# Performance work log

Measured on AMD Instinct MI355X. Metric: run time of the kernel, lower is better.

## Reference

```python
import jax, jax.numpy as jnp
import numpy as np

B, N, C_IN, C_OUT, K = 2, 8192, 128, 128, 21  # K = num_neighbors + 1 (self)
EPS = 1e-5

def knn_idx(xyz, k):
    # xyz: [B,N,3] -> idx [B,N,k] of k nearest neighbors (self included)
    d2 = jnp.sum(xyz * xyz, axis=-1)  # [B,N]
    dist = d2[:, :, None] + d2[:, None, :] - 2.0 * jnp.einsum('bnd,bmd->bnm', xyz, xyz)
    _, idx = jax.lax.top_k(-dist, k)
    return idx

def group_points(pts, idx):
    # pts [B,N,D], idx [B,N,K] -> [B,N,K,D]
    return jax.vmap(lambda p, i: p[i])(pts, idx)

def group_feats(f, idx):
    # f [B,C,N], idx [B,N,K] -> [B,C,N,K]
    return jax.vmap(lambda ff, i: ff[:, i])(f, idx)

def conv_bn_relu(x, W, g, b, m, v):
    # 1x1 conv (bias=False) + BatchNorm (inference stats) + ReLU
    y = jnp.einsum('oc,bcnk->bonk', W, x)
    inv = g / jnp.sqrt(v + EPS)
    return jax.nn.relu(y * inv[None, :, None, None] + (b - m * inv)[None, :, None, None])

def setup_inputs():
    key = jax.random.key(0)
    ks = jax.random.split(key, 12)
    return {
        'xyz': jax.random.normal(ks[0], (B, N, 3), jnp.float32),
        'f': jax.random.normal(ks[1], (B, C_IN, N), jnp.float32),
        'W_geo': jax.random.normal(ks[2], (C_OUT, 6), jnp.float32) * 0.1,
        'g_geo': jax.random.uniform(ks[3], (C_OUT,), jnp.float32, 0.5, 1.5),
        'b_geo': jax.random.normal(ks[4], (C_OUT,), jnp.float32) * 0.1,
        'm_geo': jax.random.normal(ks[5], (C_OUT,), jnp.float32) * 0.1,
        'v_geo': jax.random.uniform(ks[6], (C_OUT,), jnp.float32, 0.5, 1.5),
        'W_feat': jax.random.normal(ks[7], (C_OUT, 2 * C_IN), jnp.float32) * 0.05,
        'g_feat': jax.random.uniform(ks[8], (C_OUT,), jnp.float32, 0.5, 1.5),
        'b_feat': jax.random.normal(ks[9], (C_OUT,), jnp.float32) * 0.1,
        'm_feat': jax.random.normal(ks[10], (C_OUT,), jnp.float32) * 0.1,
        'v_feat': jax.random.uniform(ks[11], (C_OUT,), jnp.float32, 0.5, 1.5),
    }

def reference(xyz, f, W_geo, g_geo, b_geo, m_geo, v_geo, W_feat, g_feat, b_feat, m_feat, v_feat):
    idx = knn_idx(xyz, K)                                   # [B,N,K]
    grouped_xyz = group_points(xyz, idx)                    # [B,N,K,3]
    xyz_diff = jnp.transpose(grouped_xyz - xyz[:, :, None, :], (0, 3, 1, 2))  # [B,3,N,K]
    center = jnp.broadcast_to(jnp.transpose(xyz, (0, 2, 1))[:, :, :, None], (B, 3, N, K))
    G_geo = jnp.concatenate([center, xyz_diff], axis=1)     # [B,6,N,K]
    grouped_f = group_feats(f, idx)                         # [B,C,N,K]
    center_f = jnp.broadcast_to(f[:, :, :, None], (B, C_IN, N, K))
    G_feat = jnp.concatenate([center_f, grouped_f - center_f], axis=1)  # [B,2C,N,K]
    G_geo = conv_bn_relu(G_geo, W_geo, g_geo, b_geo, m_geo, v_geo)      # [B,C_OUT,N,K]
    G_feat = conv_bn_relu(G_feat, W_feat, g_feat, b_feat, m_feat, v_feat)
    feature = jnp.concatenate([G_geo, G_feat], axis=1)      # [B,2*C_OUT,N,K]
    return jnp.max(feature, axis=-1)                        # [B,2*C_OUT,N]
```

## Files before the change

kernel.cpp:

```cpp
#include <hip/hip_runtime.h>

typedef unsigned int u32;
typedef unsigned long long u64;
typedef unsigned short u16;

#define DEV __device__ __forceinline__

DEV u16 f2bf(float x) {
  u32 u = __float_as_uint(x);
  u32 r = u + 0x7fffu + ((u >> 16) & 1u);
  return (u16)(r >> 16);
}
DEV float bflo(u32 d) { return __uint_as_float(d << 16); }
DEV float bfhi(u32 d) { return __uint_as_float(d & 0xffff0000u); }
DEV u64 sortable64(double f) {
  long long b = __double_as_longlong(f);
  return (u64)b ^ (u64)((b >> 63) | (long long)0x8000000000000000ll);
}
DEV double ddist(double qx, double qy, double qz, double qd2,
                 float mxf, float myf, float mzf) {
  double cx = (double)mxf, cy = (double)myf, cz = (double)mzf;
  double cd2 = cx * cx + cy * cy + cz * cz;
  double dot = cx * qx + cy * qy + cz * qz;
  return (qd2 + cd2) - 2.0 * dot;
}

#define NB 2
#define NN 8192
#define NC 128
#define KK 21
#define MARGIN 1e-3f
#define CT 2048

__global__ __launch_bounds__(256) void k_prep(
    const float* __restrict__ Wf, const float* __restrict__ gf, const float* __restrict__ bf_,
    const float* __restrict__ mf, const float* __restrict__ vf,
    const float* __restrict__ Wg, const float* __restrict__ gg, const float* __restrict__ bg,
    const float* __restrict__ mg, const float* __restrict__ vg,
    u16* __restrict__ Wt, float* __restrict__ beta_f,
    float* __restrict__ Wgu, float* __restrict__ Wgv, float* __restrict__ beta_g) {
  int g = blockIdx.x * 256 + threadIdx.x;
  int c = g >> 8, o = g & 255;
  float val;
  if (o < 128) {
    float inv = gf[o] / sqrtf(vf[o] + 1e-5f);
    val = inv * (Wf[o * 256 + c] - Wf[o * 256 + c + 128]);
  } else {
    int o2 = o - 128;
    float inv = gf[o2] / sqrtf(vf[o2] + 1e-5f);
    val = inv * Wf[o2 * 256 + c + 128];
  }
  Wt[c * 256 + o] = f2bf(val);
  if (g < 128) {
    float inv = gf[g] / sqrtf(vf[g] + 1e-5f);
    beta_f[g] = bf_[g] - mf[g] * inv;
  } else if (g < 256) {
    int oo = g - 128;
    float invg = gg[oo] / sqrtf(vg[oo] + 1e-5f);
#pragma unroll
    for (int d = 0; d < 3; ++d) {
      Wgu[oo * 3 + d] = invg * (Wg[oo * 6 + d] - Wg[oo * 6 + 3 + d]);
      Wgv[oo * 3 + d] = invg * Wg[oo * 6 + 3 + d];
    }
    beta_g[oo] = bg[oo] - mg[oo] * invg;
  }
}

__global__ __launch_bounds__(256) void k_geo(
    const float* __restrict__ xyz, const float* __restrict__ Wgu, const float* __restrict__ Wgv,
    const float* __restrict__ beta_g, u32* __restrict__ ucat, u32* __restrict__ vcat) {
  int g = blockIdx.x * 256 + threadIdx.x;
  int p = g >> 6, oc = g & 63;
  const float* xp = xyz + p * 3;
  float X = xp[0], Y = xp[1], Z = xp[2];
  u32 du = 0, dv = 0;
#pragma unroll
  for (int h = 0; h < 2; ++h) {
    int o = oc * 2 + h;
    float ug = X * Wgu[o * 3] + Y * Wgu[o * 3 + 1] + Z * Wgu[o * 3 + 2] + beta_g[o];
    float vv = X * Wgv[o * 3] + Y * Wgv[o * 3 + 1] + Z * Wgv[o * 3 + 2];
    du |= (u32)f2bf(ug) << (16 * h);
    dv |= (u32)f2bf(vv) << (16 * h);
  }
  ucat[p * 128 + oc] = du;
  vcat[p * 128 + oc] = dv;
}

__global__ __launch_bounds__(256) void k_feat(
    const float* __restrict__ f, const u32* __restrict__ Wt32, const float* __restrict__ beta_f,
    u32* __restrict__ ucat, u32* __restrict__ vcat) {
  __shared__ u32 sW[128 * 64];
  __shared__ float sF[128][68];

  const int t = threadIdx.x;
  const int blk = blockIdx.x;
  const int H = blk & 1;
  const int b = blk >> 8;
  const int n0 = ((blk >> 1) & 127) << 6;
  const int boff = b * (NC * NN);

#pragma unroll
  for (int k = 0; k < 32; ++k) {
    int i = t + (k << 8);
    sW[i] = Wt32[((i >> 6) << 7) + (H << 6) + (i & 63)];
  }
#pragma unroll
  for (int k = 0; k < 32; ++k) {
    int i = t + (k << 8);
    int c = i >> 6, col = i & 63;
    sF[c][col] = f[boff + c * NN + n0 + col];
  }
  __syncthreads();

  const int w = t >> 6, lane = t & 63;
  const int og = lane >> 4, pg = lane & 15;
  const int o0 = (w << 5) + (og << 3);
  const int p0 = pg << 2;

  float acc[8][4];
#pragma unroll
  for (int a = 0; a < 8; ++a)
#pragma unroll
    for (int p = 0; p < 4; ++p) acc[a][p] = 0.0f;

  for (int c = 0; c < 128; ++c) {
    float4 fa = *(const float4*)&sF[c][p0];
    uint4 wr = *(const uint4*)&sW[(c << 6) + (o0 >> 1)];
    float wv[8] = {bflo(wr.x), bfhi(wr.x), bflo(wr.y), bfhi(wr.y),
                   bflo(wr.z), bfhi(wr.z), bflo(wr.w), bfhi(wr.w)};
    float fv[4] = {fa.x, fa.y, fa.z, fa.w};
#pragma unroll
    for (int a = 0; a < 8; ++a)
#pragma unroll
      for (int p = 0; p < 4; ++p) acc[a][p] = __builtin_fmaf(wv[a], fv[p], acc[a][p]);
  }

  float bet[8];
#pragma unroll
  for (int a = 0; a < 8; ++a) bet[a] = (H == 0) ? beta_f[o0 + a] : 0.0f;
  u32* dstbase = (H == 0) ? ucat : vcat;
#pragma unroll
  for (int p = 0; p < 4; ++p) {
    int pt = (b << 13) + n0 + p0 + p;
    u32 d0 = (u32)f2bf(acc[0][p] + bet[0]) | ((u32)f2bf(acc[1][p] + bet[1]) << 16);
    u32 d1 = (u32)f2bf(acc[2][p] + bet[2]) | ((u32)f2bf(acc[3][p] + bet[3]) << 16);
    u32 d2 = (u32)f2bf(acc[4][p] + bet[4]) | ((u32)f2bf(acc[5][p] + bet[5]) << 16);
    u32 d3 = (u32)f2bf(acc[6][p] + bet[6]) | ((u32)f2bf(acc[7][p] + bet[7]) << 16);
    *(uint4*)&dstbase[pt * 128 + 64 + (o0 >> 1)] = make_uint4(d0, d1, d2, d3);
  }
}

__global__ __launch_bounds__(256, 4) void k_knn(const float* __restrict__ xyz,
                                                int* __restrict__ knn) {
  __shared__ float4 sc[CT];
  __shared__ u16 ssurv[16][128];
  __shared__ u32 scnt[16];

  const int t = threadIdx.x;
  const int blk = blockIdx.x;
  const int b = blk >> 9;
  const int n0 = (blk & 511) << 4;
  const float* X = xyz + b * (NN * 3);

  if (t < 16) scnt[t] = 0u;

  const int w = t >> 6, lane = t & 63;

  float mx[4], my[4], mz[4];
#pragma unroll
  for (int i = 0; i < 4; ++i) {
    int q = n0 + (w << 2) + i;
    mx[i] = -2.0f * X[q * 3];
    my[i] = -2.0f * X[q * 3 + 1];
    mz[i] = -2.0f * X[q * 3 + 2];
  }

  float mn[4];
#pragma unroll
  for (int i = 0; i < 4; ++i) mn[i] = __builtin_inff();

  for (int ct = 0; ct < NN / CT; ++ct) {
    __syncthreads();
    const float* Xt = X + ct * (CT * 3);
#pragma unroll
    for (int k = 0; k < 8; ++k) {
      int c = (k << 8) + t;
      float x = Xt[c * 3], y = Xt[c * 3 + 1], z = Xt[c * 3 + 2];
      float d2 = __builtin_fmaf(x, x, __builtin_fmaf(y, y, z * z));
      sc[c] = make_float4(x, y, z, d2);
    }
    __syncthreads();
#pragma unroll 4
    for (int cc = 0; cc < CT; cc += 64) {
      float4 C = sc[cc + lane];
#pragma unroll
      for (int i = 0; i < 4; ++i) {
        float s = __builtin_fmaf(C.x, mx[i],
                  __builtin_fmaf(C.y, my[i],
                  __builtin_fmaf(C.z, mz[i], C.w)));
        mn[i] = fminf(mn[i], s);
      }
    }
  }

  float thr[4];
#pragma unroll
  for (int i = 0; i < 4; ++i) {
    float v = mn[i];
#pragma unroll
    for (int k = 2; k <= 64; k <<= 1) {
#pragma unroll
      for (int j = k >> 1; j > 0; j >>= 1) {
        float p = __shfl_xor(v, j);
        bool takeMin = (((lane & k) == 0) == ((lane & j) == 0));
        v = takeMin ? fminf(v, p) : fmaxf(v, p);
      }
    }
    thr[i] = __shfl(v, 20) + MARGIN;
  }

  for (int ct = 0; ct < NN / CT; ++ct) {
    __syncthreads();
    const float* Xt = X + ct * (CT * 3);
#pragma unroll
    for (int k = 0; k < 8; ++k) {
      int c = (k << 8) + t;
      float x = Xt[c * 3], y = Xt[c * 3 + 1], z = Xt[c * 3 + 2];
      float d2 = __builtin_fmaf(x, x, __builtin_fmaf(y, y, z * z));
      sc[c] = make_float4(x, y, z, d2);
    }
    __syncthreads();
    int mbase = ct * CT + lane;
#pragma unroll 4
    for (int cc = 0; cc < CT; cc += 64) {
      float4 C = sc[cc + lane];
#pragma unroll
      for (int i = 0; i < 4; ++i) {
        float s = __builtin_fmaf(C.x, mx[i],
                  __builtin_fmaf(C.y, my[i],
                  __builtin_fmaf(C.z, mz[i], C.w)));
        if (s <= thr[i]) {
          int qq = (w << 2) + i;
          u32 slot = atomicAdd(&scnt[qq], 1u);
          if (slot < 128u) ssurv[qq][slot] = (u16)(mbase + cc);
        }
      }
    }
  }
  __syncthreads();

#pragma unroll 1
  for (int i = 0; i < 4; ++i) {
    const int qq = (w << 2) + i;
    const int q = n0 + qq;
    double Qx = (double)X[q * 3], Qy = (double)X[q * 3 + 1], Qz = (double)X[q * 3 + 2];
    double Qd2 = Qx * Qx + Qy * Qy + Qz * Qz;
    u32 cnt = scnt[qq];
    int* outp = knn + ((b << 13) + q) * KK;

    bool v0 = ((u32)lane < cnt);
    u32 m0 = v0 ? (u32)ssurv[qq][lane] : 0u;
    double s0 = ddist(Qx, Qy, Qz, Qd2, X[m0 * 3], X[m0 * 3 + 1], X[m0 * 3 + 2]);
    u64 k0 = v0 ? ((sortable64(s0) & 0xFFFFFFFFFFFFE000ull) | (u64)m0) : ~0ull;

    if (cnt <= 64u) {
      u64 v = k0;
#pragma unroll
      for (int k = 2; k <= 64; k <<= 1) {
#pragma unroll
        for (int j = k >> 1; j > 0; j >>= 1) {
          u64 p = __shfl_xor(v, j);
          bool takeMin = (((lane & k) == 0) == ((lane & j) == 0));
          bool pl = p < v;
          u64 mnv = pl ? p : v;
          u64 mxv = pl ? v : p;
          v = takeMin ? mnv : mxv;
        }
      }
      if (lane < KK) outp[lane] = (int)(v & 8191ull);
    } else {
      bool v1 = ((u32)(lane + 64) < cnt);
      u32 m1 = v1 ? (u32)ssurv[qq][lane + 64] : 0u;
      double s1 = ddist(Qx, Qy, Qz, Qd2, X[m1 * 3], X[m1 * 3 + 1], X[m1 * 3 + 2]);
      u64 k1 = v1 ? ((sortable64(s1) & 0xFFFFFFFFFFFFE000ull) | (u64)m1) : ~0ull;
      u32 selm = 0;
      for (int r = 0; r < KK; ++r) {
        u64 mk = (k0 < k1) ? k0 : k1;
#pragma unroll
        for (int j = 32; j > 0; j >>= 1) {
          u64 p = __shfl_xor(mk, j);
          if (p < mk) mk = p;
        }
        if (k0 == mk) k0 = ~0ull;
        else if (k1 == mk) k1 = ~0ull;
        if (lane == r) selm = (u32)(mk & 8191ull);
      }
      if (lane < KK) outp[lane] = (int)selm;
    }
  }
}

__global__ __launch_bounds__(256) void k_gather(
    const u32* __restrict__ ucat, const u32* __restrict__ vcat,
    const int* __restrict__ knn, float* __restrict__ out) {
  __shared__ float tr[64 * 129];

  const int t = threadIdx.x;
  const int blk = blockIdx.x;
  const int H = blk & 1;
  const int b = blk >> 8;
  const int n0 = ((blk >> 1) & 127) << 6;
  const int w = t >> 6, lane = t & 63;
  const int lo = (H << 6) | lane;

  for (int step = 0; step < 16; ++step) {
    int qq = step * 4 + w;
    int q = n0 + qq;
    const int* ip = knn + ((b << 13) + q) * KK;
    float a0 = -__builtin_inff(), a1 = -__builtin_inff();
#pragma unroll
    for (int k = 0; k < KK; ++k) {
      int p = ip[k];
      u32 d = vcat[(((b << 13) + p) << 7) + lo];
      a0 = fmaxf(a0, bflo(d));
      a1 = fmaxf(a1, bfhi(d));
    }
    u32 u = ucat[(((b << 13) + q) << 7) + lo];
    float r0 = fmaxf(bflo(u) + a0, 0.0f);
    float r1 = fmaxf(bfhi(u) + a1, 0.0f);
    tr[qq * 129 + lane] = r0;
    tr[qq * 129 + 64 + lane] = r1;
  }
  __syncthreads();

  float* ob = out + b * (256 * NN) + (H << 7) * NN;
  for (int i = 0; i < 32; ++i) {
    int o = (w << 5) + i;
    int col = ((o & 1) << 6) + (o >> 1);
    ob[o * NN + n0 + lane] = tr[lane * 129 + col];
  }
}

extern "C" void kernel_launch(void* const* d_in, const int* in_sizes, int n_in,
                              void* d_out, int out_size, void* d_ws, size_t ws_size,
                              hipStream_t stream) {
  const float* xyz = (const float*)d_in[0];
  const float* f   = (const float*)d_in[1];
  const float* Wg  = (const float*)d_in[2];
  const float* gg  = (const float*)d_in[3];
  const float* bg  = (const float*)d_in[4];
  const float* mg  = (const float*)d_in[5];
  const float* vg  = (const float*)d_in[6];
  const float* Wf  = (const float*)d_in[7];
  const float* gf  = (const float*)d_in[8];
  const float* bf_ = (const float*)d_in[9];
  const float* mf  = (const float*)d_in[10];
  const float* vf  = (const float*)d_in[11];

  char* ws = (char*)d_ws;
  u16*   Wt     = (u16*)ws;
  float* beta_f = (float*)(ws + 65536);
  float* Wgu    = (float*)(ws + 66048);
  float* Wgv    = (float*)(ws + 67584);
  float* beta_g = (float*)(ws + 69120);
  u32*   ucat   = (u32*)(ws + 69632);
  u32*   vcat   = (u32*)(ws + 69632 + 8388608);
  int*   knn    = (int*)(ws + 69632 + 2 * 8388608);
  float* out    = (float*)d_out;

  if (ws_size < (size_t)(69632 + 2 * 8388608 + 16384 * KK * 4)) return;

  k_prep<<<dim3(128), dim3(256), 0, stream>>>(Wf, gf, bf_, mf, vf, Wg, gg, bg, mg, vg,
                                              Wt, beta_f, Wgu, Wgv, beta_g);
  k_geo<<<dim3(4096), dim3(256), 0, stream>>>(xyz, Wgu, Wgv, beta_g, ucat, vcat);
  k_feat<<<dim3(512), dim3(256), 0, stream>>>(f, (const u32*)Wt, beta_f, ucat, vcat);
  k_knn<<<dim3(1024), dim3(256), 0, stream>>>(xyz, knn);
  k_gather<<<dim3(512), dim3(256), 0, stream>>>(ucat, vcat, knn, out);
}
```

Baseline: 184.5 us.

## Register-prefetch next KNN candidate tile and split gather into quarter-channel blocks

In the KNN kernel, each thread now loads the next tile of candidate coordinates into registers while the current tile is written to shared memory and scanned. This hides the global-load latency behind the distance loop in both passes. The launch-bounds occupancy hint is dropped to allow the extra registers. Separately, the gather kernel now has each block handle 64 output channels instead of 128, with half-waves processing different points, and the grid is doubled. This gives more blocks and a smaller shared transpose buffer, at the cost of loading the neighbour indices twice as often.

```diff
diff --git a/kernel.cpp b/kernel.cpp
--- a/kernel.cpp
+++ b/kernel.cpp
@@ -150,8 +150,8 @@
   }
 }
 
-__global__ __launch_bounds__(256, 4) void k_knn(const float* __restrict__ xyz,
-                                                int* __restrict__ knn) {
+__global__ __launch_bounds__(256) void k_knn(const float* __restrict__ xyz,
+                                             int* __restrict__ knn) {
   __shared__ float4 sc[CT];
   __shared__ u16 ssurv[16][128];
   __shared__ u32 scnt[16];
@@ -175,19 +175,32 @@
     mz[i] = -2.0f * X[q * 3 + 2];
   }
 
+  float px[8], py[8], pz[8];
+#pragma unroll
+  for (int k = 0; k < 8; ++k) {
+    int c = (k << 8) + t;
+    px[k] = X[c * 3]; py[k] = X[c * 3 + 1]; pz[k] = X[c * 3 + 2];
+  }
+
   float mn[4];
 #pragma unroll
   for (int i = 0; i < 4; ++i) mn[i] = __builtin_inff();
 
   for (int ct = 0; ct < NN / CT; ++ct) {
     __syncthreads();
-    const float* Xt = X + ct * (CT * 3);
 #pragma unroll
     for (int k = 0; k < 8; ++k) {
       int c = (k << 8) + t;
-      float x = Xt[c * 3], y = Xt[c * 3 + 1], z = Xt[c * 3 + 2];
-      float d2 = __builtin_fmaf(x, x, __builtin_fmaf(y, y, z * z));
-      sc[c] = make_float4(x, y, z, d2);
+      float x = px[k], y = py[k], z = pz[k];
+      sc[c] = make_float4(x, y, z, __builtin_fmaf(x, x, __builtin_fmaf(y, y, z * z)));
+    }
+    if (ct < NN / CT - 1) {
+      const float* Xt = X + (ct + 1) * (CT * 3);
+#pragma unroll
+      for (int k = 0; k < 8; ++k) {
+        int c = (k << 8) + t;
+        px[k] = Xt[c * 3]; py[k] = Xt[c * 3 + 1]; pz[k] = Xt[c * 3 + 2];
+      }
     }
     __syncthreads();
 #pragma unroll 4
@@ -203,6 +216,12 @@
     }
   }
 
+#pragma unroll
+  for (int k = 0; k < 8; ++k) {
+    int c = (k << 8) + t;
+    px[k] = X[c * 3]; py[k] = X[c * 3 + 1]; pz[k] = X[c * 3 + 2];
+  }
+
   float thr[4];
 #pragma unroll
   for (int i = 0; i < 4; ++i) {
@@ -221,13 +240,19 @@
 
   for (int ct = 0; ct < NN / CT; ++ct) {
     __syncthreads();
-    const float* Xt = X + ct * (CT * 3);
 #pragma unroll
     for (int k = 0; k < 8; ++k) {
       int c = (k << 8) + t;
-      float x = Xt[c * 3], y = Xt[c * 3 + 1], z = Xt[c * 3 + 2];
-      float d2 = __builtin_fmaf(x, x, __builtin_fmaf(y, y, z * z));
-      sc[c] = make_float4(x, y, z, d2);
+      float x = px[k], y = py[k], z = pz[k];
+      sc[c] = make_float4(x, y, z, __builtin_fmaf(x, x, __builtin_fmaf(y, y, z * z)));
+    }
+    if (ct < NN / CT - 1) {
+      const float* Xt = X + (ct + 1) * (CT * 3);
+#pragma unroll
+      for (int k = 0; k < 8; ++k) {
+        int c = (k << 8) + t;
+        px[k] = Xt[c * 3]; py[k] = Xt[c * 3 + 1]; pz[k] = Xt[c * 3 + 2];
+      }
     }
     __syncthreads();
     int mbase = ct * CT + lane;
@@ -303,18 +328,20 @@
 __global__ __launch_bounds__(256) void k_gather(
     const u32* __restrict__ ucat, const u32* __restrict__ vcat,
     const int* __restrict__ knn, float* __restrict__ out) {
-  __shared__ float tr[64 * 129];
+  __shared__ float tr[64 * 65];
 
   const int t = threadIdx.x;
   const int blk = blockIdx.x;
-  const int H = blk & 1;
-  const int b = blk >> 8;
-  const int n0 = ((blk >> 1) & 127) << 6;
+  const int Q = blk & 3;
+  const int b = blk >> 9;
+  const int n0 = ((blk >> 2) & 127) << 6;
   const int w = t >> 6, lane = t & 63;
-  const int lo = (H << 6) | lane;
-
-  for (int step = 0; step < 16; ++step) {
-    int qq = step * 4 + w;
+  const int half = lane >> 5;
+  const int l32 = lane & 31;
+  const int lo = (Q << 5) | l32;
+
+  for (int step = 0; step < 8; ++step) {
+    int qq = (step << 3) + (w << 1) + half;
     int q = n0 + qq;
     const int* ip = knn + ((b << 13) + q) * KK;
     float a0 = -__builtin_inff(), a1 = -__builtin_inff();
@@ -326,18 +353,16 @@
       a1 = fmaxf(a1, bfhi(d));
     }
     u32 u = ucat[(((b << 13) + q) << 7) + lo];
-    float r0 = fmaxf(bflo(u) + a0, 0.0f);
-    float r1 = fmaxf(bfhi(u) + a1, 0.0f);
-    tr[qq * 129 + lane] = r0;
-    tr[qq * 129 + 64 + lane] = r1;
+    tr[qq * 65 + l32] = fmaxf(bflo(u) + a0, 0.0f);
+    tr[qq * 65 + 32 + l32] = fmaxf(bfhi(u) + a1, 0.0f);
   }
   __syncthreads();
 
-  float* ob = out + b * (256 * NN) + (H << 7) * NN;
-  for (int i = 0; i < 32; ++i) {
-    int o = (w << 5) + i;
-    int col = ((o & 1) << 6) + (o >> 1);
-    ob[o * NN + n0 + lane] = tr[lane * 129 + col];
+  float* ob = out + b * (256 * NN) + (Q << 6) * NN;
+  for (int i = 0; i < 16; ++i) {
+    int o = (w << 4) + i;
+    int col = ((o & 1) << 5) + (o >> 1);
+    ob[o * NN + n0 + lane] = tr[lane * 65 + col];
   }
 }
 
@@ -375,5 +400,5 @@
   k_geo<<<dim3(4096), dim3(256), 0, stream>>>(xyz, Wgu, Wgv, beta_g, ucat, vcat);
   k_feat<<<dim3(512), dim3(256), 0, stream>>>(f, (const u32*)Wt, beta_f, ucat, vcat);
   k_knn<<<dim3(1024), dim3(256), 0, stream>>>(xyz, knn);
-  k_gather<<<dim3(512), dim3(256), 0, stream>>>(ucat, vcat, knn, out);
-}
+  k_gather<<<dim3(1024), dim3(256), 0, stream>>>(ucat, vcat, knn, out);
+}
```

New measurement: 187.4 us. About the same (+1.6%).
